# Optimization experiments

Measured on AMD Instinct MI355X. Metric: run time of the kernel, lower is better.

The kernel has to match this reference:

```python
import jax, jax.numpy as jnp
import numpy as np

M, N, D, P = 1024, 4096, 128, 3072
H = N // D


def setup_inputs() -> dict:
    key = jax.random.key(0)
    ks = jax.random.split(key, 6)
    X = jax.random.normal(ks[0], (M, N), dtype=jnp.float32)
    W_q = jax.random.normal(ks[1], (N, N), dtype=jnp.float32) * 0.02
    W_k = jax.random.normal(ks[2], (N, N), dtype=jnp.float32) * 0.02
    W_v = jax.random.normal(ks[3], (N, N), dtype=jnp.float32) * 0.02
    cache_K = jax.random.normal(ks[4], (H, P, D), dtype=jnp.float32)
    cache_V = jax.random.normal(ks[5], (H, P, D), dtype=jnp.float32)
    return {"X": X, "W_q": W_q, "W_k": W_k, "W_v": W_v,
            "cache_K": cache_K, "cache_V": cache_V}


def _rms_norm(t):
    # RMS over last dim, no eps, no learned scale (matches source)
    var = jnp.mean(t * t, axis=-1, keepdims=True)
    return t * jax.lax.rsqrt(var)


def reference(X, W_q, W_k, W_v, cache_K, cache_V):
    # QKV projections: [M, N] -> [H, M, D]
    q = (X @ W_q).reshape(M, H, D).transpose(1, 0, 2)
    k = (X @ W_k).reshape(M, H, D).transpose(1, 0, 2)
    v = (X @ W_v).reshape(M, H, D).transpose(1, 0, 2)

    q = _rms_norm(q)
    k = _rms_norm(k)

    # KV-cache concat along sequence dim: [H, P+M, D]
    k_cache = jnp.concatenate([cache_K[:, :P, :], k], axis=1)
    v_cache = jnp.concatenate([cache_V[:, :P, :], v], axis=1)

    # Non-causal prefill attention, sm_scale = 1.0
    scores = jnp.einsum('hmd,hnd->hmn', q, k_cache)  # [H, M, P+M]
    attn = jax.nn.softmax(scores, axis=-1)
    out = jnp.einsum('hmn,hnd->hmd', attn, v_cache)  # [H, M, D]

    return out.transpose(1, 0, 2).reshape(M, N)
```

## Files before the change

### kernel.cpp

```cpp
#include <hip/hip_runtime.h>

#define MM 1024
#define NN 4096
#define DD 128
#define HH 32
#define PP 3072
#define LL 4096

typedef __attribute__((ext_vector_type(8))) short short8;
typedef __attribute__((ext_vector_type(4))) float f32x4;

__device__ __forceinline__ float bf2f(short b) {
  union { unsigned u; float f; } c;
  c.u = ((unsigned)(unsigned short)b) << 16;
  return c.f;
}

__device__ __forceinline__ short f2bf(float f) {
  union { float f; unsigned u; } c; c.f = f;
  unsigned r = c.u + 0x7FFFu + ((c.u >> 16) & 1u);
  return (short)(r >> 16);
}

struct bf2 { short hi, lo; };
__device__ __forceinline__ bf2 split2(float x) {
  bf2 r;
  r.hi = f2bf(x);
  r.lo = f2bf(x - bf2f(r.hi));
  return r;
}

__device__ __forceinline__ short8 cvt8(const float* __restrict__ p) {
  const f32x4 a = *(const f32x4*)p;
  const f32x4 b = *(const f32x4*)(p + 4);
  short8 r;
  r[0] = f2bf(a[0]); r[1] = f2bf(a[1]); r[2] = f2bf(a[2]); r[3] = f2bf(a[3]);
  r[4] = f2bf(b[0]); r[5] = f2bf(b[1]); r[6] = f2bf(b[2]); r[7] = f2bf(b[3]);
  return r;
}

__device__ __forceinline__ void gload16(const void* g, void* l) {
  __builtin_amdgcn_global_load_lds(
      (const __attribute__((address_space(1))) void*)g,
      (__attribute__((address_space(3))) void*)l, 16, 0, 0);
}

__global__ __launch_bounds__(256) void split_x(
    const float* __restrict__ in, short* __restrict__ oh,
    short* __restrict__ ol, int n8)
{
  int i = blockIdx.x * blockDim.x + threadIdx.x;
  if (i >= n8) return;
  const float* p = in + (size_t)i * 8;
  f32x4 a = *(const f32x4*)p, b = *(const f32x4*)(p + 4);
  short8 h, l;
  #pragma unroll
  for (int j = 0; j < 4; ++j) {
    bf2 ra = split2(a[j]); h[j] = ra.hi; l[j] = ra.lo;
    bf2 rb = split2(b[j]); h[4 + j] = rb.hi; l[4 + j] = rb.lo;
  }
  *(short8*)(oh + (size_t)i * 8) = h;
  *(short8*)(ol + (size_t)i * 8) = l;
}

__global__ __launch_bounds__(256) void split_w_t(
    const float* __restrict__ W, short* __restrict__ oh,
    short* __restrict__ ol)
{
  const int n0 = blockIdx.x * 256;
  const int k0 = blockIdx.y * 64;
  const int t  = threadIdx.x;
  const int k8 = k0 + ((t >> 5) << 3);
  const int n8 = n0 + ((t & 31) << 3);

  f32x4 xa[8], xb[8];
  #pragma unroll
  for (int r = 0; r < 8; ++r) {
    const float* p = W + (size_t)(k8 + r) * 4096 + n8;
    xa[r] = *(const f32x4*)p;
    xb[r] = *(const f32x4*)(p + 4);
  }
  #pragma unroll
  for (int c = 0; c < 8; ++c) {
    short8 th, tl;
    #pragma unroll
    for (int r = 0; r < 8; ++r) {
      float v = (c < 4) ? xa[r][c] : xb[r][c - 4];
      bf2 s = split2(v);
      th[r] = s.hi; tl[r] = s.lo;
    }
    size_t o = (size_t)(n8 + c) * 4096 + k8;
    *(short8*)(oh + o) = th;
    if (ol) *(short8*)(ol + o) = tl;
  }
}

__global__ __launch_bounds__(256) void gemm_split_bt(
    const short* __restrict__ Ah_g, const short* __restrict__ Al_g,
    const short* __restrict__ Bh_g, const short* __restrict__ Bl_g,
    float* __restrict__ O)
{
  const int n0 = blockIdx.x * 128;
  const int m0 = blockIdx.y * 128;
  const int t  = threadIdx.x;
  const int wave = t >> 6;
  const int lane = t & 63;
  const int ln   = lane & 15;
  const int quad = lane >> 4;
  const int q8   = quad * 8;
  const int wm = (wave >> 1) * 64;
  const int wn = (wave & 1) * 64;
  const int sr = lane >> 3;
  const int sc = (lane & 7) * 8;

  __shared__ short Ash[128 * 64];
  __shared__ short Asl[128 * 64];
  __shared__ short Bsh[128 * 64];
  __shared__ short Bsl[128 * 64];

  f32x4 acc[4][4];
  #pragma unroll
  for (int mi = 0; mi < 4; ++mi)
    #pragma unroll
    for (int ni = 0; ni < 4; ++ni)
      acc[mi][ni] = (f32x4){0.f, 0.f, 0.f, 0.f};

  const size_t a_base = (size_t)(m0 + wave * 32 + sr) * 4096 + sc;
  const size_t b_base = (size_t)(n0 + wave * 32 + sr) * 4096 + sc;
  const int l_base = wave * 32 * 64;

  for (int kt = 0; kt < 4096; kt += 64) {
    #pragma unroll
    for (int i = 0; i < 4; ++i) {
      size_t ao = a_base + kt + (size_t)(i * 8) * 4096;
      size_t bo = b_base + kt + (size_t)(i * 8) * 4096;
      int lo = l_base + i * 8 * 64;
      gload16(Ah_g + ao, Ash + lo);
      gload16(Al_g + ao, Asl + lo);
      gload16(Bh_g + bo, Bsh + lo);
      gload16(Bl_g + bo, Bsl + lo);
    }
    __syncthreads();
    #pragma unroll
    for (int kk = 0; kk < 64; kk += 32) {
      short8 ah[4], al[4], bh[4], bl[4];
      #pragma unroll
      for (int mi = 0; mi < 4; ++mi) {
        int ro = (wm + mi * 16 + ln) * 64 + kk + q8;
        ah[mi] = *(const short8*)(Ash + ro);
        al[mi] = *(const short8*)(Asl + ro);
      }
      #pragma unroll
      for (int ni = 0; ni < 4; ++ni) {
        int ro = (wn + ni * 16 + ln) * 64 + kk + q8;
        bh[ni] = *(const short8*)(Bsh + ro);
        bl[ni] = *(const short8*)(Bsl + ro);
      }
      #pragma unroll
      for (int ni = 0; ni < 4; ++ni)
        #pragma unroll
        for (int mi = 0; mi < 4; ++mi) {
          acc[mi][ni] = __builtin_amdgcn_mfma_f32_16x16x32_bf16(ah[mi], bh[ni], acc[mi][ni], 0, 0, 0);
          acc[mi][ni] = __builtin_amdgcn_mfma_f32_16x16x32_bf16(ah[mi], bl[ni], acc[mi][ni], 0, 0, 0);
          acc[mi][ni] = __builtin_amdgcn_mfma_f32_16x16x32_bf16(al[mi], bh[ni], acc[mi][ni], 0, 0, 0);
        }
    }
    __syncthreads();
  }

  #pragma unroll
  for (int mi = 0; mi < 4; ++mi)
    #pragma unroll
    for (int ni = 0; ni < 4; ++ni)
      #pragma unroll
      for (int r = 0; r < 4; ++r) {
        int row = m0 + wm + mi * 16 + quad * 4 + r;
        int col = n0 + wn + ni * 16 + ln;
        O[(size_t)row * 4096 + col] = acc[mi][ni][r];
      }
}

__global__ __launch_bounds__(256) void gemm_bf16_bt(
    const short* __restrict__ Ah_g, const short* __restrict__ Bh_g,
    short* __restrict__ Ov)
{
  const int n0 = blockIdx.x * 128;
  const int m0 = blockIdx.y * 128;
  const int t  = threadIdx.x;
  const int wave = t >> 6;
  const int lane = t & 63;
  const int ln   = lane & 15;
  const int quad = lane >> 4;
  const int q8   = quad * 8;
  const int wm = (wave >> 1) * 64;
  const int wn = (wave & 1) * 64;
  const int sr = lane >> 3;
  const int sc = (lane & 7) * 8;

  __shared__ short Ash[128 * 64];
  __shared__ short Bsh[128 * 64];

  f32x4 acc[4][4];
  #pragma unroll
  for (int mi = 0; mi < 4; ++mi)
    #pragma unroll
    for (int ni = 0; ni < 4; ++ni)
      acc[mi][ni] = (f32x4){0.f, 0.f, 0.f, 0.f};

  const size_t a_base = (size_t)(m0 + wave * 32 + sr) * 4096 + sc;
  const size_t b_base = (size_t)(n0 + wave * 32 + sr) * 4096 + sc;
  const int l_base = wave * 32 * 64;

  for (int kt = 0; kt < 4096; kt += 64) {
    #pragma unroll
    for (int i = 0; i < 4; ++i) {
      size_t ao = a_base + kt + (size_t)(i * 8) * 4096;
      size_t bo = b_base + kt + (size_t)(i * 8) * 4096;
      int lo = l_base + i * 8 * 64;
      gload16(Ah_g + ao, Ash + lo);
      gload16(Bh_g + bo, Bsh + lo);
    }
    __syncthreads();
    #pragma unroll
    for (int kk = 0; kk < 64; kk += 32) {
      short8 ah[4], bh[4];
      #pragma unroll
      for (int mi = 0; mi < 4; ++mi)
        ah[mi] = *(const short8*)(Ash + (wm + mi * 16 + ln) * 64 + kk + q8);
      #pragma unroll
      for (int ni = 0; ni < 4; ++ni)
        bh[ni] = *(const short8*)(Bsh + (wn + ni * 16 + ln) * 64 + kk + q8);
      #pragma unroll
      for (int ni = 0; ni < 4; ++ni)
        #pragma unroll
        for (int mi = 0; mi < 4; ++mi)
          acc[mi][ni] = __builtin_amdgcn_mfma_f32_16x16x32_bf16(ah[mi], bh[ni], acc[mi][ni], 0, 0, 0);
    }
    __syncthreads();
  }

  #pragma unroll
  for (int mi = 0; mi < 4; ++mi)
    #pragma unroll
    for (int ni = 0; ni < 4; ++ni)
      #pragma unroll
      for (int r = 0; r < 4; ++r) {
        int row = m0 + wm + mi * 16 + quad * 4 + r;
        int col = n0 + wn + ni * 16 + ln;
        Ov[(size_t)row * 4096 + col] = f2bf(acc[mi][ni][r]);
      }
}

__global__ __launch_bounds__(256) void rmsnorm_f32(
    float* __restrict__ Q, float* __restrict__ K)
{
  float* __restrict__ buf = (blockIdx.y == 0) ? Q : K;
  const int m = blockIdx.x;
  const int t = threadIdx.x;
  const int head = t >> 3, li = t & 7;
  size_t base = (size_t)m * 4096 + head * 128 + li * 16;

  f32x4 a[4];
  float ss = 0.f;
  #pragma unroll
  for (int i = 0; i < 4; ++i) {
    a[i] = *(const f32x4*)(buf + base + i * 4);
    #pragma unroll
    for (int j = 0; j < 4; ++j) ss += a[i][j] * a[i][j];
  }
  #pragma unroll
  for (int d = 1; d < 8; d <<= 1) ss += __shfl_xor(ss, d, 64);
  float scale = rsqrtf(ss * (1.0f / 128.0f));
  #pragma unroll
  for (int i = 0; i < 4; ++i) {
    #pragma unroll
    for (int j = 0; j < 4; ++j) a[i][j] *= scale;
    *(f32x4*)(buf + base + i * 4) = a[i];
  }
}

__global__ __launch_bounds__(256) void prep_k(
    const float* __restrict__ Kf, const float* __restrict__ cK,
    short* __restrict__ Khi, short* __restrict__ Klo)
{
  const int h  = blockIdx.y;
  const int k0 = blockIdx.x * 64;
  const int t  = threadIdx.x;
  const int d0 = (t & 7) * 16;
  #pragma unroll
  for (int i = 0; i < 2; ++i) {
    int key = k0 + i * 32 + (t >> 3);
    const float* src = (key < PP)
        ? cK + ((size_t)h * PP + key) * 128 + d0
        : Kf + (size_t)(key - PP) * 4096 + h * 128 + d0;
    f32x4 x0 = *(const f32x4*)src,       x1 = *(const f32x4*)(src + 4);
    f32x4 x2 = *(const f32x4*)(src + 8), x3 = *(const f32x4*)(src + 12);
    short8 h0, l0, h1, l1;
    #pragma unroll
    for (int j = 0; j < 4; ++j) {
      bf2 r0 = split2(x0[j]); h0[j] = r0.hi; l0[j] = r0.lo;
      bf2 r1 = split2(x1[j]); h0[4 + j] = r1.hi; l0[4 + j] = r1.lo;
      bf2 r2 = split2(x2[j]); h1[j] = r2.hi; l1[j] = r2.lo;
      bf2 r3 = split2(x3[j]); h1[4 + j] = r3.hi; l1[4 + j] = r3.lo;
    }
    size_t row = ((size_t)h * 4096 + key) * 128;
    int s  = key & 7;
    int b0 = (t & 7) * 2, b1 = b0 + 1;
    *(short8*)(Khi + row + ((b0 ^ s) << 3)) = h0;
    *(short8*)(Khi + row + ((b1 ^ s) << 3)) = h1;
    *(short8*)(Klo + row + ((b0 ^ s) << 3)) = l0;
    *(short8*)(Klo + row + ((b1 ^ s) << 3)) = l1;
  }
}

__global__ __launch_bounds__(256) void prep_v(
    const short* __restrict__ Vb, const float* __restrict__ cV,
    short* __restrict__ Vtt)
{
  const int h    = blockIdx.y;
  const int k0   = blockIdx.x * 128;
  const int t    = threadIdx.x;
  const int kb_g = (k0 >> 3) + (t >> 4);
  const int db   = t & 15;
  const int key0 = kb_g * 8;

  short8 row[8];
  if (key0 < PP) {
    #pragma unroll
    for (int r = 0; r < 8; ++r)
      row[r] = cvt8(cV + ((size_t)h * PP + key0 + r) * 128 + db * 8);
  } else {
    #pragma unroll
    for (int r = 0; r < 8; ++r)
      row[r] = *(const short8*)(Vb + (size_t)(key0 + r - PP) * 4096 + h * 128 + db * 8);
  }

  const int tile = kb_g >> 3, kbt = kb_g & 7;
  size_t tb = ((size_t)h * 64 + tile) * 8192;
  #pragma unroll
  for (int c = 0; c < 8; ++c) {
    int d = db * 8 + c;
    short8 o;
    #pragma unroll
    for (int r = 0; r < 8; ++r) o[r] = row[r][c];
    *(short8*)(Vtt + tb + d * 64 + ((kbt ^ c) << 3)) = o;
  }
}

__global__ __launch_bounds__(256) void attn(
    const float* __restrict__ Qf,
    const short* __restrict__ Khi,
    const short* __restrict__ Klo,
    const short* __restrict__ Vtt,
    float* __restrict__ Out)
{
  const int h  = blockIdx.y;
  const int m0 = blockIdx.x * 64;
  const int t  = threadIdx.x;
  const int w    = t >> 6;
  const int lane = t & 63;
  const int ln   = lane & 15;
  const int quad = lane >> 4;
  const int q8   = quad * 8;

  __shared__ short k_hi[64 * 128];
  __shared__ short k_lo[64 * 128];
  __shared__ short v_t[128 * 64];
  __shared__ short p_s[64 * 72];
  __shared__ float a_l[64], l_l[64];

  short8 qh[4], ql[4];
  {
    int qrow = m0 + w * 16 + ln;
    #pragma unroll
    for (int dc = 0; dc < 4; ++dc) {
      const float* qp = Qf + (size_t)qrow * 4096 + h * 128 + dc * 32 + q8;
      f32x4 a = *(const f32x4*)qp, b = *(const f32x4*)(qp + 4);
      #pragma unroll
      for (int j = 0; j < 4; ++j) {
        bf2 ra = split2(a[j]); qh[dc][j] = ra.hi; ql[dc][j] = ra.lo;
        bf2 rb = split2(b[j]); qh[dc][4 + j] = rb.hi; ql[dc][4 + j] = rb.lo;
      }
    }
  }

  float m_st[4], l_st[4];
  #pragma unroll
  for (int r = 0; r < 4; ++r) { m_st[r] = -1e30f; l_st[r] = 0.f; }

  f32x4 oacc[4][2];
  #pragma unroll
  for (int ms = 0; ms < 4; ++ms)
    #pragma unroll
    for (int i = 0; i < 2; ++i)
      oacc[ms][i] = (f32x4){0.f, 0.f, 0.f, 0.f};

  const size_t khead = (size_t)h * 4096 * 128;
  const size_t vhead = (size_t)h * 64 * 8192;

  for (int kb = 0; kb < LL; kb += 64) {
    const size_t kt = khead + (size_t)kb * 128;
    const size_t vt = vhead + (size_t)(kb >> 6) * 8192;
    #pragma unroll
    for (int i = 0; i < 4; ++i) {
      int lo = i * 2048 + w * 512;
      gload16(Khi + kt + lo + lane * 8, k_hi + lo);
      gload16(Klo + kt + lo + lane * 8, k_lo + lo);
      gload16(Vtt + vt + lo + lane * 8, v_t + lo);
    }
    __syncthreads();

    f32x4 sacc[4];
    #pragma unroll
    for (int ni = 0; ni < 4; ++ni) sacc[ni] = (f32x4){0.f, 0.f, 0.f, 0.f};
    __builtin_amdgcn_s_setprio(1);
    #pragma unroll
    for (int ni = 0; ni < 4; ++ni) {
      const int r = ni * 16 + ln;
      #pragma unroll
      for (int dc = 0; dc < 4; ++dc) {
        int ro = r * 128 + (((dc * 4 + quad) ^ (r & 7)) << 3);
        short8 kh = *(const short8*)(k_hi + ro);
        short8 kl = *(const short8*)(k_lo + ro);
        sacc[ni] = __builtin_amdgcn_mfma_f32_16x16x32_bf16(qh[dc], kh, sacc[ni], 0, 0, 0);
        sacc[ni] = __builtin_amdgcn_mfma_f32_16x16x32_bf16(qh[dc], kl, sacc[ni], 0, 0, 0);
        sacc[ni] = __builtin_amdgcn_mfma_f32_16x16x32_bf16(ql[dc], kh, sacc[ni], 0, 0, 0);
      }
    }
    __builtin_amdgcn_s_setprio(0);

    float alpha[4];
    #pragma unroll
    for (int rr = 0; rr < 4; ++rr) {
      float mx = fmaxf(fmaxf(sacc[0][rr], sacc[1][rr]),
                       fmaxf(sacc[2][rr], sacc[3][rr]));
      #pragma unroll
      for (int d = 1; d < 16; d <<= 1) mx = fmaxf(mx, __shfl_xor(mx, d, 64));
      float mn = fmaxf(m_st[rr], mx);
      alpha[rr] = __expf(m_st[rr] - mn);
      float p0 = __expf(sacc[0][rr] - mn);
      float p1 = __expf(sacc[1][rr] - mn);
      float p2 = __expf(sacc[2][rr] - mn);
      float p3 = __expf(sacc[3][rr] - mn);
      float s = p0 + p1 + p2 + p3;
      #pragma unroll
      for (int d = 1; d < 16; d <<= 1) s += __shfl_xor(s, d, 64);
      l_st[rr] = l_st[rr] * alpha[rr] + s;
      m_st[rr] = mn;
      int prow = (w * 16 + quad * 4 + rr) * 72;
      p_s[prow + 0 * 16 + ln] = f2bf(p0);
      p_s[prow + 1 * 16 + ln] = f2bf(p1);
      p_s[prow + 2 * 16 + ln] = f2bf(p2);
      p_s[prow + 3 * 16 + ln] = f2bf(p3);
    }
    if (ln == 0) {
      #pragma unroll
      for (int rr = 0; rr < 4; ++rr) a_l[w * 16 + quad * 4 + rr] = alpha[rr];
    }
    __syncthreads();

    #pragma unroll
    for (int ms = 0; ms < 4; ++ms) {
      f32x4 av = *(const f32x4*)(a_l + ms * 16 + quad * 4);
      #pragma unroll
      for (int i = 0; i < 2; ++i)
        #pragma unroll
        for (int r = 0; r < 4; ++r) oacc[ms][i][r] *= av[r];
    }
    #pragma unroll
    for (int kk = 0; kk < 64; kk += 32) {
      short8 vf[2];
      #pragma unroll
      for (int i = 0; i < 2; ++i) {
        int d = (w * 2 + i) * 16 + ln;
        int ro = d * 64 + ((((kk + q8) >> 3) ^ (d & 7)) << 3);
        vf[i] = *(const short8*)(v_t + ro);
      }
      __builtin_amdgcn_s_setprio(1);
      #pragma unroll
      for (int ms = 0; ms < 4; ++ms) {
        short8 pf = *(const short8*)(p_s + (ms * 16 + ln) * 72 + kk + q8);
        #pragma unroll
        for (int i = 0; i < 2; ++i)
          oacc[ms][i] = __builtin_amdgcn_mfma_f32_16x16x32_bf16(pf, vf[i], oacc[ms][i], 0, 0, 0);
      }
      __builtin_amdgcn_s_setprio(0);
    }
    __syncthreads();
  }

  if (ln == 0) {
    #pragma unroll
    for (int rr = 0; rr < 4; ++rr) l_l[w * 16 + quad * 4 + rr] = l_st[rr];
  }
  __syncthreads();

  #pragma unroll
  for (int ms = 0; ms < 4; ++ms) {
    f32x4 lv = *(const f32x4*)(l_l + ms * 16 + quad * 4);
    #pragma unroll
    for (int i = 0; i < 2; ++i) {
      int col = h * 128 + (w * 2 + i) * 16 + ln;
      #pragma unroll
      for (int r = 0; r < 4; ++r) {
        int row = m0 + ms * 16 + quad * 4 + r;
        Out[(size_t)row * 4096 + col] = oacc[ms][i][r] / lv[r];
      }
    }
  }
}

extern "C" void kernel_launch(void* const* d_in, const int* in_sizes, int n_in,
                              void* d_out, int out_size, void* d_ws, size_t ws_size,
                              hipStream_t stream) {
  const float* X  = (const float*)d_in[0];
  const float* Wq = (const float*)d_in[1];
  const float* Wk = (const float*)d_in[2];
  const float* Wv = (const float*)d_in[3];
  const float* cK = (const float*)d_in[4];
  const float* cV = (const float*)d_in[5];
  float* out = (float*)d_out;

  const size_t MB = 1u << 20;
  char* w = (char*)d_ws;
  float* Qf  = (float*)(w);
  float* Kf  = (float*)(w + 16 * MB);
  short* Xh  = (short*)(w + 32 * MB);
  short* Xl  = (short*)(w + 40 * MB);
  short* Vb  = (short*)(w + 48 * MB);
  short* Wth = (short*)(w + 56 * MB);
  short* Wtl = (short*)(w + 88 * MB);
  short* Khi = (short*)(w + 56 * MB);
  short* Klo = (short*)(w + 88 * MB);
  short* Vtt = (short*)(w + 16 * MB);

  {
    int n8 = (int)((size_t)MM * NN / 8);
    split_x<<<n8 / 256, 256, 0, stream>>>(X, Xh, Xl, n8);
  }

  dim3 gw(NN / 256, NN / 64);
  dim3 gg(NN / 128, MM / 128);

  split_w_t<<<gw, 256, 0, stream>>>(Wq, Wth, Wtl);
  gemm_split_bt<<<gg, 256, 0, stream>>>(Xh, Xl, Wth, Wtl, Qf);

  split_w_t<<<gw, 256, 0, stream>>>(Wk, Wth, Wtl);
  gemm_split_bt<<<gg, 256, 0, stream>>>(Xh, Xl, Wth, Wtl, Kf);

  split_w_t<<<gw, 256, 0, stream>>>(Wv, Wth, nullptr);
  gemm_bf16_bt<<<gg, 256, 0, stream>>>(Xh, Wth, Vb);

  dim3 gn(MM, 2);
  rmsnorm_f32<<<gn, 256, 0, stream>>>(Qf, Kf);

  dim3 gk(LL / 64, HH);
  prep_k<<<gk, 256, 0, stream>>>(Kf, cK, Khi, Klo);
  dim3 gv(LL / 128, HH);
  prep_v<<<gv, 256, 0, stream>>>(Vb, cV, Vtt);

  dim3 ga(MM / 64, HH);
  attn<<<ga, 256, 0, stream>>>(Qf, Khi, Klo, Vtt, out);
}
```

Measured before the change: 918.7 us.

## Fuse RMS norm into prep_k and attn, double-buffer K/V tiles, widen query tile

The standalone rmsnorm kernel is removed. K normalization now happens inside prep_k for the new keys, and Q normalization happens when the attention kernel loads Q. The attention kernel now processes 128 query rows per block, with each wave owning 32 rows and the full D dimension. This removes the cross-wave alpha exchange through shared memory and one barrier per iteration. K/V tiles are double-buffered so the next tile's global-to-LDS load overlaps compute, at the cost of more LDS and registers (launch bounds set to one block) and half as many blocks.

```diff
diff --git a/kernel.cpp b/kernel.cpp
--- a/kernel.cpp
+++ b/kernel.cpp
@@ -251,34 +251,6 @@
       }
 }
 
-__global__ __launch_bounds__(256) void rmsnorm_f32(
-    float* __restrict__ Q, float* __restrict__ K)
-{
-  float* __restrict__ buf = (blockIdx.y == 0) ? Q : K;
-  const int m = blockIdx.x;
-  const int t = threadIdx.x;
-  const int head = t >> 3, li = t & 7;
-  size_t base = (size_t)m * 4096 + head * 128 + li * 16;
-
-  f32x4 a[4];
-  float ss = 0.f;
-  #pragma unroll
-  for (int i = 0; i < 4; ++i) {
-    a[i] = *(const f32x4*)(buf + base + i * 4);
-    #pragma unroll
-    for (int j = 0; j < 4; ++j) ss += a[i][j] * a[i][j];
-  }
-  #pragma unroll
-  for (int d = 1; d < 8; d <<= 1) ss += __shfl_xor(ss, d, 64);
-  float scale = rsqrtf(ss * (1.0f / 128.0f));
-  #pragma unroll
-  for (int i = 0; i < 4; ++i) {
-    #pragma unroll
-    for (int j = 0; j < 4; ++j) a[i][j] *= scale;
-    *(f32x4*)(buf + base + i * 4) = a[i];
-  }
-}
-
 __global__ __launch_bounds__(256) void prep_k(
     const float* __restrict__ Kf, const float* __restrict__ cK,
     short* __restrict__ Khi, short* __restrict__ Klo)
@@ -290,11 +262,26 @@
   #pragma unroll
   for (int i = 0; i < 2; ++i) {
     int key = k0 + i * 32 + (t >> 3);
-    const float* src = (key < PP)
+    const bool isnew = (key >= PP);
+    const float* src = !isnew
         ? cK + ((size_t)h * PP + key) * 128 + d0
         : Kf + (size_t)(key - PP) * 4096 + h * 128 + d0;
     f32x4 x0 = *(const f32x4*)src,       x1 = *(const f32x4*)(src + 4);
     f32x4 x2 = *(const f32x4*)(src + 8), x3 = *(const f32x4*)(src + 12);
+    if (isnew) {
+      float ss = 0.f;
+      #pragma unroll
+      for (int j = 0; j < 4; ++j)
+        ss += x0[j]*x0[j] + x1[j]*x1[j] + x2[j]*x2[j] + x3[j]*x3[j];
+      ss += __shfl_xor(ss, 1, 64);
+      ss += __shfl_xor(ss, 2, 64);
+      ss += __shfl_xor(ss, 4, 64);
+      float sc = rsqrtf(ss * (1.0f / 128.0f));
+      #pragma unroll
+      for (int j = 0; j < 4; ++j) {
+        x0[j] *= sc; x1[j] *= sc; x2[j] *= sc; x3[j] *= sc;
+      }
+    }
     short8 h0, l0, h1, l1;
     #pragma unroll
     for (int j = 0; j < 4; ++j) {
@@ -347,7 +334,7 @@
   }
 }
 
-__global__ __launch_bounds__(256) void attn(
+__global__ __launch_bounds__(256, 1) void attn(
     const float* __restrict__ Qf,
     const short* __restrict__ Khi,
     const short* __restrict__ Klo,
@@ -355,7 +342,7 @@
     float* __restrict__ Out)
 {
   const int h  = blockIdx.y;
-  const int m0 = blockIdx.x * 64;
+  const int m0 = blockIdx.x * 128;
   const int t  = threadIdx.x;
   const int w    = t >> 6;
   const int lane = t & 63;
@@ -363,56 +350,91 @@
   const int quad = lane >> 4;
   const int q8   = quad * 8;
 
-  __shared__ short k_hi[64 * 128];
-  __shared__ short k_lo[64 * 128];
-  __shared__ short v_t[128 * 64];
-  __shared__ short p_s[64 * 72];
-  __shared__ float a_l[64], l_l[64];
-
-  short8 qh[4], ql[4];
-  {
-    int qrow = m0 + w * 16 + ln;
+  __shared__ short k_hi[2 * 64 * 128];
+  __shared__ short k_lo[2 * 64 * 128];
+  __shared__ short v_t[2 * 128 * 64];
+  __shared__ short p_s[128 * 72];
+
+  short8 qh[2][4], ql[2][4];
+  #pragma unroll
+  for (int mi = 0; mi < 2; ++mi) {
+    int qrow = m0 + w * 32 + mi * 16 + ln;
+    f32x4 xa[4], xb[4];
+    float ss = 0.f;
     #pragma unroll
     for (int dc = 0; dc < 4; ++dc) {
       const float* qp = Qf + (size_t)qrow * 4096 + h * 128 + dc * 32 + q8;
-      f32x4 a = *(const f32x4*)qp, b = *(const f32x4*)(qp + 4);
+      xa[dc] = *(const f32x4*)qp;
+      xb[dc] = *(const f32x4*)(qp + 4);
+      #pragma unroll
+      for (int j = 0; j < 4; ++j)
+        ss += xa[dc][j] * xa[dc][j] + xb[dc][j] * xb[dc][j];
+    }
+    ss += __shfl_xor(ss, 16, 64);
+    ss += __shfl_xor(ss, 32, 64);
+    float scale = rsqrtf(ss * (1.0f / 128.0f));
+    #pragma unroll
+    for (int dc = 0; dc < 4; ++dc) {
       #pragma unroll
       for (int j = 0; j < 4; ++j) {
-        bf2 ra = split2(a[j]); qh[dc][j] = ra.hi; ql[dc][j] = ra.lo;
-        bf2 rb = split2(b[j]); qh[dc][4 + j] = rb.hi; ql[dc][4 + j] = rb.lo;
-      }
-    }
-  }
-
-  float m_st[4], l_st[4];
-  #pragma unroll
-  for (int r = 0; r < 4; ++r) { m_st[r] = -1e30f; l_st[r] = 0.f; }
-
-  f32x4 oacc[4][2];
-  #pragma unroll
-  for (int ms = 0; ms < 4; ++ms)
-    #pragma unroll
-    for (int i = 0; i < 2; ++i)
-      oacc[ms][i] = (f32x4){0.f, 0.f, 0.f, 0.f};
+        bf2 ra = split2(xa[dc][j] * scale);
+        qh[mi][dc][j] = ra.hi; ql[mi][dc][j] = ra.lo;
+        bf2 rb = split2(xb[dc][j] * scale);
+        qh[mi][dc][4 + j] = rb.hi; ql[mi][dc][4 + j] = rb.lo;
+      }
+    }
+  }
+
+  float m_st[2][4], l_st[2][4];
+  #pragma unroll
+  for (int mi = 0; mi < 2; ++mi)
+    #pragma unroll
+    for (int r = 0; r < 4; ++r) { m_st[mi][r] = -1e30f; l_st[mi][r] = 0.f; }
+
+  f32x4 oacc[2][8];
+  #pragma unroll
+  for (int mi = 0; mi < 2; ++mi)
+    #pragma unroll
+    for (int ds = 0; ds < 8; ++ds)
+      oacc[mi][ds] = (f32x4){0.f, 0.f, 0.f, 0.f};
 
   const size_t khead = (size_t)h * 4096 * 128;
   const size_t vhead = (size_t)h * 64 * 8192;
 
-  for (int kb = 0; kb < LL; kb += 64) {
-    const size_t kt = khead + (size_t)kb * 128;
-    const size_t vt = vhead + (size_t)(kb >> 6) * 8192;
-    #pragma unroll
-    for (int i = 0; i < 4; ++i) {
-      int lo = i * 2048 + w * 512;
-      gload16(Khi + kt + lo + lane * 8, k_hi + lo);
-      gload16(Klo + kt + lo + lane * 8, k_lo + lo);
-      gload16(Vtt + vt + lo + lane * 8, v_t + lo);
-    }
-    __syncthreads();
-
-    f32x4 sacc[4];
-    #pragma unroll
-    for (int ni = 0; ni < 4; ++ni) sacc[ni] = (f32x4){0.f, 0.f, 0.f, 0.f};
+  #pragma unroll
+  for (int i = 0; i < 4; ++i) {
+    int lo = i * 2048 + w * 512;
+    gload16(Khi + khead + lo + lane * 8, k_hi + lo);
+    gload16(Klo + khead + lo + lane * 8, k_lo + lo);
+    gload16(Vtt + vhead + lo + lane * 8, v_t + lo);
+  }
+  __syncthreads();
+
+  for (int it = 0; it < 64; ++it) {
+    const int cur = it & 1;
+    const short* khb = k_hi + cur * 8192;
+    const short* klb = k_lo + cur * 8192;
+    const short* vtb = v_t  + cur * 8192;
+
+    if (it < 63) {
+      const size_t kt = khead + (size_t)(it + 1) * 8192;
+      const size_t vt = vhead + (size_t)(it + 1) * 8192;
+      const int bb = (1 - cur) * 8192;
+      #pragma unroll
+      for (int i = 0; i < 4; ++i) {
+        int lo = i * 2048 + w * 512;
+        gload16(Khi + kt + lo + lane * 8, k_hi + bb + lo);
+        gload16(Klo + kt + lo + lane * 8, k_lo + bb + lo);
+        gload16(Vtt + vt + lo + lane * 8, v_t + bb + lo);
+      }
+    }
+
+    f32x4 sacc[2][4];
+    #pragma unroll
+    for (int mi = 0; mi < 2; ++mi)
+      #pragma unroll
+      for (int ni = 0; ni < 4; ++ni)
+        sacc[mi][ni] = (f32x4){0.f, 0.f, 0.f, 0.f};
     __builtin_amdgcn_s_setprio(1);
     #pragma unroll
     for (int ni = 0; ni < 4; ++ni) {
@@ -420,91 +442,86 @@
       #pragma unroll
       for (int dc = 0; dc < 4; ++dc) {
         int ro = r * 128 + (((dc * 4 + quad) ^ (r & 7)) << 3);
-        short8 kh = *(const short8*)(k_hi + ro);
-        short8 kl = *(const short8*)(k_lo + ro);
-        sacc[ni] = __builtin_amdgcn_mfma_f32_16x16x32_bf16(qh[dc], kh, sacc[ni], 0, 0, 0);
-        sacc[ni] = __builtin_amdgcn_mfma_f32_16x16x32_bf16(qh[dc], kl, sacc[ni], 0, 0, 0);
-        sacc[ni] = __builtin_amdgcn_mfma_f32_16x16x32_bf16(ql[dc], kh, sacc[ni], 0, 0, 0);
+        short8 kh = *(const short8*)(khb + ro);
+        short8 kl = *(const short8*)(klb + ro);
+        #pragma unroll
+        for (int mi = 0; mi < 2; ++mi) {
+          sacc[mi][ni] = __builtin_amdgcn_mfma_f32_16x16x32_bf16(qh[mi][dc], kh, sacc[mi][ni], 0, 0, 0);
+          sacc[mi][ni] = __builtin_amdgcn_mfma_f32_16x16x32_bf16(qh[mi][dc], kl, sacc[mi][ni], 0, 0, 0);
+          sacc[mi][ni] = __builtin_amdgcn_mfma_f32_16x16x32_bf16(ql[mi][dc], kh, sacc[mi][ni], 0, 0, 0);
+        }
       }
     }
     __builtin_amdgcn_s_setprio(0);
 
-    float alpha[4];
-    #pragma unroll
-    for (int rr = 0; rr < 4; ++rr) {
-      float mx = fmaxf(fmaxf(sacc[0][rr], sacc[1][rr]),
-                       fmaxf(sacc[2][rr], sacc[3][rr]));
-      #pragma unroll
-      for (int d = 1; d < 16; d <<= 1) mx = fmaxf(mx, __shfl_xor(mx, d, 64));
-      float mn = fmaxf(m_st[rr], mx);
-      alpha[rr] = __expf(m_st[rr] - mn);
-      float p0 = __expf(sacc[0][rr] - mn);
-      float p1 = __expf(sacc[1][rr] - mn);
-      float p2 = __expf(sacc[2][rr] - mn);
-      float p3 = __expf(sacc[3][rr] - mn);
-      float s = p0 + p1 + p2 + p3;
-      #pragma unroll
-      for (int d = 1; d < 16; d <<= 1) s += __shfl_xor(s, d, 64);
-      l_st[rr] = l_st[rr] * alpha[rr] + s;
-      m_st[rr] = mn;
-      int prow = (w * 16 + quad * 4 + rr) * 72;
-      p_s[prow + 0 * 16 + ln] = f2bf(p0);
-      p_s[prow + 1 * 16 + ln] = f2bf(p1);
-      p_s[prow + 2 * 16 + ln] = f2bf(p2);
-      p_s[prow + 3 * 16 + ln] = f2bf(p3);
-    }
-    if (ln == 0) {
-      #pragma unroll
-      for (int rr = 0; rr < 4; ++rr) a_l[w * 16 + quad * 4 + rr] = alpha[rr];
-    }
+    float alpha[2][4];
+    #pragma unroll
+    for (int mi = 0; mi < 2; ++mi) {
+      #pragma unroll
+      for (int rr = 0; rr < 4; ++rr) {
+        float mx = fmaxf(fmaxf(sacc[mi][0][rr], sacc[mi][1][rr]),
+                         fmaxf(sacc[mi][2][rr], sacc[mi][3][rr]));
+        #pragma unroll
+        for (int d = 1; d < 16; d <<= 1) mx = fmaxf(mx, __shfl_xor(mx, d, 64));
+        float mn = fmaxf(m_st[mi][rr], mx);
+        alpha[mi][rr] = __expf(m_st[mi][rr] - mn);
+        float p0 = __expf(sacc[mi][0][rr] - mn);
+        float p1 = __expf(sacc[mi][1][rr] - mn);
+        float p2 = __expf(sacc[mi][2][rr] - mn);
+        float p3 = __expf(sacc[mi][3][rr] - mn);
+        float s = p0 + p1 + p2 + p3;
+        #pragma unroll
+        for (int d = 1; d < 16; d <<= 1) s += __shfl_xor(s, d, 64);
+        l_st[mi][rr] = l_st[mi][rr] * alpha[mi][rr] + s;
+        m_st[mi][rr] = mn;
+        int prow = (w * 32 + mi * 16 + quad * 4 + rr) * 72;
+        p_s[prow + 0 * 16 + ln] = f2bf(p0);
+        p_s[prow + 1 * 16 + ln] = f2bf(p1);
+        p_s[prow + 2 * 16 + ln] = f2bf(p2);
+        p_s[prow + 3 * 16 + ln] = f2bf(p3);
+      }
+    }
+
+    #pragma unroll
+    for (int mi = 0; mi < 2; ++mi)
+      #pragma unroll
+      for (int ds = 0; ds < 8; ++ds)
+        #pragma unroll
+        for (int r = 0; r < 4; ++r)
+          oacc[mi][ds][r] *= alpha[mi][r];
+
+    #pragma unroll
+    for (int kk = 0; kk < 64; kk += 32) {
+      short8 vf[8];
+      #pragma unroll
+      for (int ds = 0; ds < 8; ++ds) {
+        int d = ds * 16 + ln;
+        int ro = d * 64 + ((((kk + q8) >> 3) ^ (d & 7)) << 3);
+        vf[ds] = *(const short8*)(vtb + ro);
+      }
+      __builtin_amdgcn_s_setprio(1);
+      #pragma unroll
+      for (int mi = 0; mi < 2; ++mi) {
+        short8 pf = *(const short8*)(p_s + (w * 32 + mi * 16 + ln) * 72 + kk + q8);
+        #pragma unroll
+        for (int ds = 0; ds < 8; ++ds)
+          oacc[mi][ds] = __builtin_amdgcn_mfma_f32_16x16x32_bf16(pf, vf[ds], oacc[mi][ds], 0, 0, 0);
+      }
+      __builtin_amdgcn_s_setprio(0);
+    }
+
     __syncthreads();
-
-    #pragma unroll
-    for (int ms = 0; ms < 4; ++ms) {
-      f32x4 av = *(const f32x4*)(a_l + ms * 16 + quad * 4);
-      #pragma unroll
-      for (int i = 0; i < 2; ++i)
-        #pragma unroll
-        for (int r = 0; r < 4; ++r) oacc[ms][i][r] *= av[r];
-    }
-    #pragma unroll
-    for (int kk = 0; kk < 64; kk += 32) {
-      short8 vf[2];
-      #pragma unroll
-      for (int i = 0; i < 2; ++i) {
-        int d = (w * 2 + i) * 16 + ln;
-        int ro = d * 64 + ((((kk + q8) >> 3) ^ (d & 7)) << 3);
-        vf[i] = *(const short8*)(v_t + ro);
-      }
-      __builtin_amdgcn_s_setprio(1);
-      #pragma unroll
-      for (int ms = 0; ms < 4; ++ms) {
-        short8 pf = *(const short8*)(p_s + (ms * 16 + ln) * 72 + kk + q8);
-        #pragma unroll
-        for (int i = 0; i < 2; ++i)
-          oacc[ms][i] = __builtin_amdgcn_mfma_f32_16x16x32_bf16(pf, vf[i], oacc[ms][i], 0, 0, 0);
-      }
-      __builtin_amdgcn_s_setprio(0);
-    }
-    __syncthreads();
-  }
-
-  if (ln == 0) {
-    #pragma unroll
-    for (int rr = 0; rr < 4; ++rr) l_l[w * 16 + quad * 4 + rr] = l_st[rr];
-  }
-  __syncthreads();
-
-  #pragma unroll
-  for (int ms = 0; ms < 4; ++ms) {
-    f32x4 lv = *(const f32x4*)(l_l + ms * 16 + quad * 4);
-    #pragma unroll
-    for (int i = 0; i < 2; ++i) {
-      int col = h * 128 + (w * 2 + i) * 16 + ln;
+  }
+
+  #pragma unroll
+  for (int mi = 0; mi < 2; ++mi) {
+    #pragma unroll
+    for (int ds = 0; ds < 8; ++ds) {
+      int col = h * 128 + ds * 16 + ln;
       #pragma unroll
       for (int r = 0; r < 4; ++r) {
-        int row = m0 + ms * 16 + quad * 4 + r;
-        Out[(size_t)row * 4096 + col] = oacc[ms][i][r] / lv[r];
+        int row = m0 + w * 32 + mi * 16 + quad * 4 + r;
+        Out[(size_t)row * 4096 + col] = oacc[mi][ds][r] / l_st[mi][r];
       }
     }
   }
@@ -551,14 +568,11 @@
   split_w_t<<<gw, 256, 0, stream>>>(Wv, Wth, nullptr);
   gemm_bf16_bt<<<gg, 256, 0, stream>>>(Xh, Wth, Vb);
 
-  dim3 gn(MM, 2);
-  rmsnorm_f32<<<gn, 256, 0, stream>>>(Qf, Kf);
-
   dim3 gk(LL / 64, HH);
   prep_k<<<gk, 256, 0, stream>>>(Kf, cK, Khi, Klo);
   dim3 gv(LL / 128, HH);
   prep_v<<<gv, 256, 0, stream>>>(Vb, cV, Vtt);
 
-  dim3 ga(MM / 64, HH);
+  dim3 ga(MM / 128, HH);
   attn<<<ga, 256, 0, stream>>>(Qf, Khi, Klo, Vtt, out);
 }
```

Measured after the change: 948.2 us. 1.03x slower.
